# Optimization experiments

Hardware: AMD Instinct MI355X
Metric: run time of the kernel (lower is better)

Reference implementation:

```python
import jax, jax.numpy as jnp
import numpy as np

# dims
B, C, N, T = 8, 64, 500, 12      # batch, channels (c_in=c_out=nhid), nodes, time
H, F = 4, 64                      # nheads, nhid per head
GDEP = 2
ALPHA = 0.05                      # mixprop residual mix
LEAK = 0.2                        # leakyrelu slope in attention


def setup_inputs() -> dict:
    key = jax.random.key(0)
    ks = jax.random.split(key, 9)
    x = jax.random.normal(ks[0], (B, C, N, T), jnp.float32)
    adj = (jax.random.uniform(ks[1], (N, N)) < 0.05).astype(jnp.float32)
    # per-head GAT params stacked on head axis
    W = jax.random.normal(ks[2], (H, C, F), jnp.float32) * 0.05   # head projection
    a1 = jax.random.normal(ks[3], (H, F), jnp.float32) * 0.05     # a[:F]
    a2 = jax.random.normal(ks[4], (H, F), jnp.float32) * 0.05     # a[F:]
    # GAT output mlp: Conv2d 1x1, (H*F) -> F
    Wg = jax.random.normal(ks[5], (F, H * F), jnp.float32) * 0.05
    bg = jnp.zeros((F,), jnp.float32)
    # mixprop mlp: (GDEP+1)*C -> C
    Wm = jax.random.normal(ks[6], (C, (GDEP + 1) * C), jnp.float32) * 0.05
    bm = jnp.zeros((C,), jnp.float32)
    return {"x": x, "adj": adj, "W": W, "a1": a1, "a2": a2,
            "Wg": Wg, "bg": bg, "Wm": Wm, "bm": bm}


def _gat(h, mask, W, a1, a2, Wg, bg):
    # h: [B,C,N,T]; eval mode (dropout = identity)
    hp = jnp.transpose(h, (0, 3, 2, 1))                 # [B,T,N,C]
    Wh = jnp.einsum('btnc,hcf->bhtnf', hp, W)           # [B,H,T,N,F]
    e1 = jnp.einsum('bhtnf,hf->bhtn', Wh, a1)           # src term
    e2 = jnp.einsum('bhtnf,hf->bhtn', Wh, a2)           # dst term
    e = jax.nn.leaky_relu(e1[..., :, None] + e2[..., None, :], LEAK)  # [B,H,T,N,N]
    e = jnp.where(mask, e, jnp.float32(-9e15))
    att = jax.nn.softmax(e, axis=-1)
    hpr = jax.nn.elu(jnp.einsum('bhtnm,bhtmf->bhtnf', att, Wh))       # [B,H,T,N,F]
    # concat heads along channel dim -> [B, H*F, N, T]
    cat = jnp.transpose(hpr, (0, 1, 4, 3, 2)).reshape(B, H * F, N, T)
    # 1x1 conv mix
    return jnp.einsum('bcnt,oc->bont', cat, Wg) + bg[None, :, None, None]


def reference(x, adj, W, a1, a2, Wg, bg, Wm, bm):
    mask = (adj + jnp.eye(N, dtype=adj.dtype)) > 0      # self-loops added
    h = x
    outs = [h]
    for _ in range(GDEP):
        h = ALPHA * x + (1.0 - ALPHA) * _gat(h, mask, W, a1, a2, Wg, bg)
        outs.append(h)
    ho = jnp.concatenate(outs, axis=1)                  # [B,(GDEP+1)*C,N,T]
    return jnp.einsum('bcnt,oc->bont', ho, Wm) + bm[None, :, None, None]
```

## Files before the change

### kernel.cpp

```cpp
#include <hip/hip_runtime.h>
#include <hip/hip_bf16.h>
#include <math.h>

#define BB 8
#define CC 64
#define NN 500
#define TT 12
#define HH 4
#define FF 64
#define CT (CC*TT)
#define HF (HH*FF)
#define NBT (HH*TT)
#define NBHT (BB*NBT)
#define NROWS (BB*HH*TT*NN)
#define NNODE (BB*NN)
#define BSR 200
#define KST 68

typedef unsigned short ushort_t;
typedef unsigned int uint_t;
typedef __attribute__((ext_vector_type(8))) short short8;
typedef __attribute__((ext_vector_type(4))) float floatx4;

static __device__ __forceinline__ ushort_t f2bf(float v) {
    __hip_bfloat16 h = __float2bfloat16(v);
    ushort_t u;
    __builtin_memcpy(&u, &h, 2);
    return u;
}

static __device__ __forceinline__ uint_t pkbf(float a, float b) {
    __hip_bfloat162 h = __float22bfloat162_rn(make_float2(a, b));
    uint_t u;
    __builtin_memcpy(&u, &h, 4);
    return u;
}

__global__ __launch_bounds__(256) void k016_setup(const float* __restrict__ adj,
                                                  const float* __restrict__ W,
                                                  const float* __restrict__ a1,
                                                  const float* __restrict__ a2,
                                                  const float* __restrict__ Wm,
                                                  const float* __restrict__ Wg,
                                                  const float* __restrict__ x,
                                                  uint_t* __restrict__ maskbits,
                                                  float* __restrict__ p1,
                                                  float* __restrict__ p2,
                                                  ushort_t* __restrict__ WmB,
                                                  ushort_t* __restrict__ WgB,
                                                  ushort_t* __restrict__ WtB,
                                                  float* __restrict__ xT) {
    __shared__ float tile[16*776];
    int blk = blockIdx.x;
    if (blk < 32) {
        int idx = blk * 256 + threadIdx.x;
        int n = idx >> 4, j = idx & 15;
        uint_t v = 0;
        if (n < NN) {
            int m0 = j * 32;
            for (int i = 0; i < 32; ++i) {
                int m = m0 + i;
                bool p = (m < NN) && (adj[n*NN + m] > 0.f || m == n);
                v |= (p ? 1u : 0u) << i;
            }
        }
        maskbits[idx] = v;
        return;
    }
    if (blk < 209) {
        int idx = (blk - 32) * 256 + threadIdx.x;
        if (idx < HH*CC) {
            int h = idx / CC, c = idx % CC;
            float s1 = 0.f, s2 = 0.f;
            for (int f = 0; f < FF; ++f) {
                float w = W[(h*CC + c)*FF + f];
                s1 += w * a1[h*FF + f];
                s2 += w * a2[h*FF + f];
            }
            p1[idx] = s1; p2[idx] = s2;
        }
        int j = idx - HH*CC;
        if (j >= 0 && j < CC*3*CC) {
            WmB[j] = f2bf(Wm[j]);
        }
        int j2 = idx - (HH*CC + CC*3*CC);
        if (j2 >= 0 && j2 < FF*HF) {
            WgB[j2] = f2bf(Wg[j2]);
        }
        int j3 = idx - (HH*CC + CC*3*CC + FF*HF);
        if (j3 >= 0 && j3 < HH*CC*FF) {
            int h = j3 >> 12, rem = j3 & 4095;
            int f = rem >> 6, c = rem & 63;
            WtB[j3] = f2bf(W[h*4096 + c*64 + f]);
        }
        return;
    }
    int xblk = blk - 209;
    int b  = xblk >> 5;
    int n0 = (xblk & 31) * 16;
    for (int idx = threadIdx.x; idx < CC*16*TT; idx += 256) {
        int c   = idx / (16*TT);
        int rem = idx % (16*TT);
        int nl  = rem / TT;
        int t   = rem % TT;
        int n   = n0 + nl;
        if (n < NN)
            tile[nl*776 + c*TT + t] = x[((b*CC + c)*NN + n)*TT + t];
    }
    __syncthreads();
    for (int idx = threadIdx.x; idx < 16*CT; idx += 256) {
        int nl = idx / CT;
        int j  = idx % CT;
        int n  = n0 + nl;
        if (n < NN)
            xT[(size_t)(b*NN + n)*CT + j] = tile[nl*776 + j];
    }
}

__global__ __launch_bounds__(256) void k2_wh_e(const float* __restrict__ hin,
                                               const ushort_t* __restrict__ WtB,
                                               const float* __restrict__ p1,
                                               const float* __restrict__ p2,
                                               ushort_t* __restrict__ Wh,
                                               float* __restrict__ e1,
                                               float* __restrict__ e2) {
    __shared__ float    hL[4][CT];
    __shared__ ushort_t Bs[4][TT*KST];
    int tid  = threadIdx.x;
    int wid  = tid >> 6;
    int lane = tid & 63;
    int quad = lane >> 4;
    int r    = lane & 15;
    int node0 = blockIdx.x * 4;

    for (int u = 0; u < 4; ++u) {
        const float4* src = (const float4*)(hin + (size_t)(node0 + u) * CT);
        float4* dst = (float4*)hL[u];
        for (int i = tid; i < CT/4; i += 256) dst[i] = src[i];
    }
    __syncthreads();
    for (int e = tid; e < 4*CT; e += 256) {
        int u = e / CT, i = e % CT;
        int c = i / TT, t = i % TT;
        Bs[u][t*KST + c] = f2bf(hL[u][i]);
    }
    __syncthreads();

    short8 Afr[4][2];
    #pragma unroll
    for (int mt = 0; mt < 4; ++mt)
        #pragma unroll
        for (int kc = 0; kc < 2; ++kc)
            Afr[mt][kc] = *(const short8*)(WtB + wid*4096 +
                                           (mt*16 + r)*64 + kc*32 + quad*8);

    int rcl = r < TT ? r : TT-1;

    for (int u = 0; u < 4; ++u) {
        floatx4 C[4];
        #pragma unroll
        for (int mt = 0; mt < 4; ++mt) C[mt] = (floatx4){0.f,0.f,0.f,0.f};
        #pragma unroll
        for (int kc = 0; kc < 2; ++kc) {
            short8 bfr = *(const short8*)&Bs[u][rcl*KST + kc*32 + quad*8];
            #pragma unroll
            for (int mt = 0; mt < 4; ++mt)
                C[mt] = __builtin_amdgcn_mfma_f32_16x16x32_bf16(Afr[mt][kc], bfr, C[mt], 0, 0, 0);
        }
        if (r < TT) {
            int node = node0 + u;
            int bb = node / NN, nn = node % NN;
            size_t row = ((size_t)((bb*HH + wid)*TT + r)*NN + nn)*FF;
            #pragma unroll
            for (int mt = 0; mt < 4; ++mt) {
                int f0 = mt*16 + quad*4;
                *(uint_t*)&Wh[row + f0]     = pkbf(C[mt][0], C[mt][1]);
                *(uint_t*)&Wh[row + f0 + 2] = pkbf(C[mt][2], C[mt][3]);
            }
        }
    }

    int t2 = lane & 15;
    if (t2 < TT) {
        int h2 = lane >> 4;
        const float* hLw = hL[wid];
        float s1 = 0.f, s2 = 0.f;
        for (int c = 0; c < CC; ++c) {
            float v = hLw[c*TT + t2];
            s1 += v * p1[h2*CC + c];
            s2 += v * p2[h2*CC + c];
        }
        int node = node0 + wid;
        int bb = node / NN, nn = node % NN;
        int idx = ((bb*HH + h2)*TT + t2)*NN + nn;
        e1[idx] = s1;
        e2[idx] = s2;
    }
}

__global__ __launch_bounds__(256) void k2t(const ushort_t* __restrict__ Wh,
                                           ushort_t* __restrict__ WhT) {
    __shared__ ushort_t tile[32*512];
    int wid  = threadIdx.x >> 6;
    int lane = threadIdx.x & 63;
    int bht  = blockIdx.x >> 1;
    int fh   = blockIdx.x & 1;
    const ushort_t* src = Wh + (size_t)bht * NN * FF + fh*32;

    for (int task = wid; task < 32; task += 4) {
        int i  = task >> 2;
        int fo = task & 3;
        int m  = i*64 + lane;
        short8 v = {0,0,0,0,0,0,0,0};
        if (m < NN) v = *(const short8*)(src + m*FF + fo*8);
        #pragma unroll
        for (int j = 0; j < 8; ++j)
            tile[(fo*8 + j)*512 + m] = (ushort_t)v[j];
    }
    __syncthreads();

    ushort_t* dst = WhT + (size_t)bht * 64 * 512 + (size_t)fh*32*512;
    for (int f = wid; f < 32; f += 4) {
        short8 v = *(const short8*)&tile[f*512 + lane*8];
        *(short8*)(dst + f*512 + lane*8) = v;
    }
}

__global__ __launch_bounds__(256, 3) void k3_attn(const ushort_t* __restrict__ WhT,
                                                  const float* __restrict__ e1,
                                                  const float* __restrict__ e2,
                                                  const uint_t* __restrict__ maskbits,
                                                  ushort_t* __restrict__ hprB) {
    __shared__ float  e2s[512];
    __shared__ uint_t mks[256*17];
    int tid  = threadIdx.x;
    int wid  = tid >> 6;
    int lane = tid & 63;
    int bht  = blockIdx.x >> 1;
    int half = blockIdx.x & 1;
    int b    = bht / NBT;
    int ht   = bht % NBT;

    const float* e1p = e1 + (size_t)bht * NN;
    const float* e2p = e2 + (size_t)bht * NN;
    const ushort_t* WT = WhT + (size_t)bht * 64 * 512;
    const float L2E = 1.4426950408889634f;

    {
        int i = tid;
        e2s[i] = (i < NN) ? e2p[i] * L2E : 0.f;
        i = tid + 256;
        e2s[i] = (i < NN) ? e2p[i] * L2E : 0.f;
    }
    for (int i = tid; i < 256*16; i += 256) {
        int rl = i >> 4, dw = i & 15;
        mks[rl*17 + dw] = maskbits[(half*256 + rl)*16 + dw];
    }
    __syncthreads();

    int quad = lane >> 4;
    int r    = lane & 15;

    const short8 ONES = {0x3F80,0x3F80,0x3F80,0x3F80,
                         0x3F80,0x3F80,0x3F80,0x3F80};

    float e1v[4];
    #pragma unroll
    for (int u = 0; u < 4; ++u) {
        int nrow = half*256 + (wid*4 + u)*16 + r;
        e1v[u] = ((nrow < NN) ? e1p[nrow] : 0.f) * L2E;
    }
    int rl0 = wid*64 + r;

    const ushort_t* WTr = WT + (size_t)r * 512;

    floatx4 C[4][4];
    floatx4 Cs[4];
    #pragma unroll
    for (int u = 0; u < 4; ++u) {
        Cs[u] = (floatx4){0.f,0.f,0.f,0.f};
        #pragma unroll
        for (int ft = 0; ft < 4; ++ft) C[u][ft] = (floatx4){0.f,0.f,0.f,0.f};
    }

    #pragma unroll
    for (int ki = 0; ki < 16; ++ki) {
        int kb = ki*32 + quad*8;

        short8 b0 = *(const short8*)(WTr + 0*8192 + kb);
        short8 b1 = *(const short8*)(WTr + 1*8192 + kb);
        short8 b2 = *(const short8*)(WTr + 2*8192 + kb);
        short8 b3 = *(const short8*)(WTr + 3*8192 + kb);

        float4 ea = *(const float4*)&e2s[kb];
        float4 eb = *(const float4*)&e2s[kb + 4];
        float ev[8] = {ea.x,ea.y,ea.z,ea.w, eb.x,eb.y,eb.z,eb.w};

        #pragma unroll
        for (int u = 0; u < 4; ++u) {
            uint_t md    = mks[(rl0 + u*16)*17 + ki];
            uint_t mbits = md >> (quad*8);
            union { uint_t w[4]; short8 s; } av;
            #pragma unroll
            for (int p = 0; p < 4; ++p) {
                float s0 = e1v[u] + ev[2*p];
                float s1 = e1v[u] + ev[2*p+1];
                float g0 = fmaxf(s0, 0.2f*s0);
                float g1 = fmaxf(s1, 0.2f*s1);
                float x0 = __builtin_amdgcn_exp2f(g0);
                float x1 = __builtin_amdgcn_exp2f(g1);
                x0 = (mbits & (1u << (2*p)))     ? x0 : 0.f;
                x1 = (mbits & (1u << (2*p + 1))) ? x1 : 0.f;
                av.w[p] = pkbf(x0, x1);
            }
            C[u][0] = __builtin_amdgcn_mfma_f32_16x16x32_bf16(av.s, b0, C[u][0], 0, 0, 0);
            C[u][1] = __builtin_amdgcn_mfma_f32_16x16x32_bf16(av.s, b1, C[u][1], 0, 0, 0);
            C[u][2] = __builtin_amdgcn_mfma_f32_16x16x32_bf16(av.s, b2, C[u][2], 0, 0, 0);
            C[u][3] = __builtin_amdgcn_mfma_f32_16x16x32_bf16(av.s, b3, C[u][3], 0, 0, 0);
            Cs[u]   = __builtin_amdgcn_mfma_f32_16x16x32_bf16(av.s, ONES, Cs[u], 0, 0, 0);
        }
    }

    #pragma unroll
    for (int u = 0; u < 4; ++u) {
        int n0 = half*256 + (wid*4 + u)*16;
        #pragma unroll
        for (int reg = 0; reg < 4; ++reg) {
            int n = n0 + quad*4 + reg;
            if (n < NN) {
                float inv = 1.0f / Cs[u][reg];
                size_t base = ((size_t)(b*NN + n)*NBT + ht)*FF;
                #pragma unroll
                for (int ft = 0; ft < 4; ++ft) {
                    float v = C[u][ft][reg] * inv;
                    v = v > 0.f ? v : __expf(v) - 1.f;
                    hprB[base + ft*16 + r] = f2bf(v);
                }
            }
        }
    }
}

__global__ __launch_bounds__(256) void k4_mfma(const ushort_t* __restrict__ hprB,
                                               const ushort_t* __restrict__ WgB,
                                               const float* __restrict__ bg,
                                               const float* __restrict__ xT,
                                               float* __restrict__ hnext) {
    __shared__ float S[4][CT];
    int wid  = threadIdx.x >> 6;
    int lane = threadIdx.x & 63;
    int quad = lane >> 4;
    int r    = lane & 15;

    short8 Afr[4][8];
    #pragma unroll
    for (int ot = 0; ot < 4; ++ot)
        #pragma unroll
        for (int kc = 0; kc < 8; ++kc)
            Afr[ot][kc] = *(const short8*)(WgB + (size_t)(ot*16 + r)*HF + kc*32 + quad*8);

    float4 bgv[4];
    #pragma unroll
    for (int ot = 0; ot < 4; ++ot)
        bgv[ot] = *(const float4*)(bg + ot*16 + quad*4);

    int tcl = r < TT ? r : TT-1;

    int node = blockIdx.x*4 + wid;
    const ushort_t* P = hprB + (size_t)node * (NBT*FF);

    floatx4 C[4];
    #pragma unroll
    for (int ot = 0; ot < 4; ++ot) C[ot] = (floatx4){0.f,0.f,0.f,0.f};

    #pragma unroll
    for (int kc = 0; kc < 8; ++kc) {
        int k = kc*32 + quad*8;
        int h = k >> 6, f0 = k & 63;
        short8 bfr = *(const short8*)(P + (h*TT + tcl)*FF + f0);
        #pragma unroll
        for (int ot = 0; ot < 4; ++ot)
            C[ot] = __builtin_amdgcn_mfma_f32_16x16x32_bf16(Afr[ot][kc], bfr, C[ot], 0, 0, 0);
    }

    if (r < TT) {
        #pragma unroll
        for (int ot = 0; ot < 4; ++ot) {
            #pragma unroll
            for (int reg = 0; reg < 4; ++reg) {
                int o = ot*16 + quad*4 + reg;
                S[wid][o*TT + r] = C[ot][reg] + bgv[ot][reg];
            }
        }
    }
    {
        const float4* xp4 = (const float4*)(xT + (size_t)node * CT);
        float4* ho4 = (float4*)(hnext + (size_t)node * CT);
        const float4* S4 = (const float4*)S[wid];
        #pragma unroll
        for (int j = 0; j < 3; ++j) {
            int i = lane + j*64;
            float4 xv = xp4[i];
            float4 sv = S4[i];
            float4 ov;
            ov.x = 0.05f*xv.x + 0.95f*sv.x;
            ov.y = 0.05f*xv.y + 0.95f*sv.y;
            ov.z = 0.05f*xv.z + 0.95f*sv.z;
            ov.w = 0.05f*xv.w + 0.95f*sv.w;
            ho4[i] = ov;
        }
    }
}

__global__ __launch_bounds__(256) void k45_fused(const ushort_t* __restrict__ hprB,
                                                 const ushort_t* __restrict__ WgB,
                                                 const float* __restrict__ bg,
                                                 const float* __restrict__ xT,
                                                 const float* __restrict__ h1,
                                                 const ushort_t* __restrict__ WmB,
                                                 const float* __restrict__ bm,
                                                 float* __restrict__ out) {
    __shared__ ushort_t Bs[4][TT*BSR];
    __shared__ float    So[4][CT];
    int wid  = threadIdx.x >> 6;
    int lane = threadIdx.x & 63;
    int quad = lane >> 4;
    int r    = lane & 15;

    int node = blockIdx.x*4 + wid;
    ushort_t* Bw = Bs[wid];

    {
        const float* xp = xT + (size_t)node*CT + lane*TT;
        const float* hp = h1 + (size_t)node*CT + lane*TT;
        float4 x0 = *(const float4*)(xp);
        float4 x1 = *(const float4*)(xp + 4);
        float4 x2 = *(const float4*)(xp + 8);
        float4 g0 = *(const float4*)(hp);
        float4 g1 = *(const float4*)(hp + 4);
        float4 g2 = *(const float4*)(hp + 8);
        float xa[12] = {x0.x,x0.y,x0.z,x0.w, x1.x,x1.y,x1.z,x1.w,
                        x2.x,x2.y,x2.z,x2.w};
        float ha[12] = {g0.x,g0.y,g0.z,g0.w, g1.x,g1.y,g1.z,g1.w,
                        g2.x,g2.y,g2.z,g2.w};
        #pragma unroll
        for (int t = 0; t < TT; ++t) {
            Bw[t*BSR + lane]      = f2bf(xa[t]);
            Bw[t*BSR + 64 + lane] = f2bf(ha[t]);
        }
    }

    {
        short8 Afr[4][8];
        #pragma unroll
        for (int ot = 0; ot < 4; ++ot)
            #pragma unroll
            for (int kc = 0; kc < 8; ++kc)
                Afr[ot][kc] = *(const short8*)(WgB + (size_t)(ot*16 + r)*HF + kc*32 + quad*8);
        float4 bgv[4];
        #pragma unroll
        for (int ot = 0; ot < 4; ++ot)
            bgv[ot] = *(const float4*)(bg + ot*16 + quad*4);

        int tcl = r < TT ? r : TT-1;
        const ushort_t* P = hprB + (size_t)node * (NBT*FF);

        floatx4 C[4];
        #pragma unroll
        for (int ot = 0; ot < 4; ++ot) C[ot] = (floatx4){0.f,0.f,0.f,0.f};
        #pragma unroll
        for (int kc = 0; kc < 8; ++kc) {
            int k = kc*32 + quad*8;
            int h = k >> 6, f0 = k & 63;
            short8 bfr = *(const short8*)(P + (h*TT + tcl)*FF + f0);
            #pragma unroll
            for (int ot = 0; ot < 4; ++ot)
                C[ot] = __builtin_amdgcn_mfma_f32_16x16x32_bf16(Afr[ot][kc], bfr, C[ot], 0, 0, 0);
        }

        if (r < TT) {
            const float* xp = xT + (size_t)node * CT;
            #pragma unroll
            for (int ot = 0; ot < 4; ++ot) {
                #pragma unroll
                for (int rp = 0; rp < 4; rp += 2) {
                    int o = ot*16 + quad*4 + rp;
                    float v0 = C[ot][rp]   + bgv[ot][rp];
                    float v1 = C[ot][rp+1] + bgv[ot][rp+1];
                    float h20 = 0.05f*xp[o*TT + r]       + 0.95f*v0;
                    float h21 = 0.05f*xp[(o+1)*TT + r]   + 0.95f*v1;
                    *(uint_t*)&Bw[r*BSR + 128 + o] = pkbf(h20, h21);
                }
            }
        }
    }

    {
        short8 Am[4][6];
        #pragma unroll
        for (int ot = 0; ot < 4; ++ot)
            #pragma unroll
            for (int kc = 0; kc < 6; ++kc)
                Am[ot][kc] = *(const short8*)(WmB + (size_t)(ot*16 + r)*(3*CC) + kc*32 + quad*8);

        int trd = r < TT ? r : TT-1;
        floatx4 C2[4];
        #pragma unroll
        for (int ot = 0; ot < 4; ++ot) C2[ot] = (floatx4){0.f,0.f,0.f,0.f};
        #pragma unroll
        for (int kc = 0; kc < 6; ++kc) {
            short8 bfr = *(const short8*)&Bw[trd*BSR + kc*32 + quad*8];
            #pragma unroll
            for (int ot = 0; ot < 4; ++ot)
                C2[ot] = __builtin_amdgcn_mfma_f32_16x16x32_bf16(Am[ot][kc], bfr, C2[ot], 0, 0, 0);
        }

        if (r < TT) {
            #pragma unroll
            for (int ot = 0; ot < 4; ++ot) {
                float4 bmv = *(const float4*)(bm + ot*16 + quad*4);
                #pragma unroll
                for (int reg = 0; reg < 4; ++reg) {
                    int o = ot*16 + quad*4 + reg;
                    So[wid][o*TT + r] = C2[ot][reg] + bmv[reg];
                }
            }
        }
    }
    __syncthreads();

    {
        int o = threadIdx.x >> 2;
        int q = threadIdx.x & 3;
        int nodeq = blockIdx.x*4 + q;
        int bq = nodeq / NN, nq = nodeq % NN;
        float* op = out + ((size_t)(bq*CC + o)*NN + nq)*TT;
        const float* Sp = So[q] + o*TT;
        *(float4*)&op[0] = *(const float4*)&Sp[0];
        *(float4*)&op[4] = *(const float4*)&Sp[4];
        *(float4*)&op[8] = *(const float4*)&Sp[8];
    }
}

extern "C" void kernel_launch(void* const* d_in, const int* in_sizes, int n_in,
                              void* d_out, int out_size, void* d_ws, size_t ws_size,
                              hipStream_t stream) {
    const float* x   = (const float*)d_in[0];
    const float* adj = (const float*)d_in[1];
    const float* W   = (const float*)d_in[2];
    const float* a1  = (const float*)d_in[3];
    const float* a2  = (const float*)d_in[4];
    const float* Wg  = (const float*)d_in[5];
    const float* bg  = (const float*)d_in[6];
    const float* Wm  = (const float*)d_in[7];
    const float* bm  = (const float*)d_in[8];
    float* out = (float*)d_out;

    char* ws = (char*)d_ws;
    size_t off = 0;
    auto alloc = [&](size_t bytes) -> void* {
        void* p = ws + off;
        off += (bytes + 255) & ~(size_t)255;
        return p;
    };

    uint_t* maskbits = (uint_t*)alloc((size_t)512 * 16 * 4);
    float* p1   = (float*)alloc(HH*CC * sizeof(float));
    float* p2   = (float*)alloc(HH*CC * sizeof(float));
    ushort_t* WmB = (ushort_t*)alloc((size_t)CC*3*CC * 2);
    ushort_t* WgB = (ushort_t*)alloc((size_t)FF*HF * 2);
    ushort_t* WtB = (ushort_t*)alloc((size_t)HH*CC*FF * 2);
    float* xT   = (float*)alloc((size_t)NNODE * CT * sizeof(float));
    ushort_t* Wh   = (ushort_t*)alloc((size_t)NROWS * FF * 2);
    ushort_t* WhT  = (ushort_t*)alloc((size_t)NBHT * 64 * 512 * 2);
    ushort_t* hprB = (ushort_t*)alloc((size_t)NNODE * NBT * FF * 2);
    float* e1   = (float*)alloc((size_t)NROWS * sizeof(float));
    float* e2   = (float*)alloc((size_t)NROWS * sizeof(float));
    float* h1   = (float*)alloc((size_t)NNODE * CT * sizeof(float));
    (void)ws_size;

    k016_setup<<<465, 256, 0, stream>>>(adj, W, a1, a2, Wm, Wg, x,
                                        maskbits, p1, p2, WmB, WgB, WtB, xT);

    k2_wh_e <<<NNODE/4, 256, 0, stream>>>(xT, WtB, p1, p2, Wh, e1, e2);
    k2t     <<<NBHT*2,  256, 0, stream>>>(Wh, WhT);
    k3_attn <<<NBHT*2,  256, 0, stream>>>(WhT, e1, e2, maskbits, hprB);
    k4_mfma <<<NNODE/4, 256, 0, stream>>>(hprB, WgB, bg, xT, h1);

    k2_wh_e <<<NNODE/4, 256, 0, stream>>>(h1, WtB, p1, p2, Wh, e1, e2);
    k2t     <<<NBHT*2,  256, 0, stream>>>(Wh, WhT);
    k3_attn <<<NBHT*2,  256, 0, stream>>>(WhT, e1, e2, maskbits, hprB);

    k45_fused<<<NNODE/4, 256, 0, stream>>>(hprB, WgB, bg, xT, h1, WmB, bm, out);
}
```

Before: 304.8 us.

## Fuse Wh transpose into projection kernel, writing transposed WhT directly

The projection kernel now handles 8 nodes per block within one batch and stages its MFMA results in shared memory in transposed [t][f][node] order. It then writes 16-byte chunks straight into the node-contiguous WhT layout, so the separate k2t transpose kernel and the intermediate Wh buffer are gone. This removes one launch and a global round trip of Wh per GAT layer. The setup kernel zeroes the WhT padding columns (500..511) once. In exchange, shared-memory use per block grows and the e1/e2 dot products are moved before the MFMA phase.

After: 303.2 us. No clear change (-0.5%).

```diff
diff --git a/kernel.cpp b/kernel.cpp
--- a/kernel.cpp
+++ b/kernel.cpp
@@ -16,6 +16,7 @@
 #define NNODE (BB*NN)
 #define BSR 200
 #define KST 68
+#define WTS 520
 
 typedef unsigned short ushort_t;
 typedef unsigned int uint_t;
@@ -49,7 +50,8 @@
                                                   ushort_t* __restrict__ WmB,
                                                   ushort_t* __restrict__ WgB,
                                                   ushort_t* __restrict__ WtB,
-                                                  float* __restrict__ xT) {
+                                                  float* __restrict__ xT,
+                                                  ushort_t* __restrict__ WhT) {
     __shared__ float tile[16*776];
     int blk = blockIdx.x;
     if (blk < 32) {
@@ -95,6 +97,13 @@
         }
         return;
     }
+    if (blk >= 465) {
+        int row = (blk - 465) * 256 + threadIdx.x;
+        uint_t* p = (uint_t*)(WhT + (size_t)row * 512 + 500);
+        #pragma unroll
+        for (int j = 0; j < 6; ++j) p[j] = 0;
+        return;
+    }
     int xblk = blk - 209;
     int b  = xblk >> 5;
     int n0 = (xblk & 31) * 16;
@@ -121,30 +130,56 @@
                                                const ushort_t* __restrict__ WtB,
                                                const float* __restrict__ p1,
                                                const float* __restrict__ p2,
-                                               ushort_t* __restrict__ Wh,
+                                               ushort_t* __restrict__ WhT,
                                                float* __restrict__ e1,
                                                float* __restrict__ e2) {
-    __shared__ float    hL[4][CT];
-    __shared__ ushort_t Bs[4][TT*KST];
+    __shared__ char uni[4*TT*WTS*2];
+    __shared__ ushort_t Bs[8][TT*KST];
+    float (*hL)[CT] = (float(*)[CT])uni;
     int tid  = threadIdx.x;
     int wid  = tid >> 6;
     int lane = tid & 63;
     int quad = lane >> 4;
     int r    = lane & 15;
-    int node0 = blockIdx.x * 4;
-
-    for (int u = 0; u < 4; ++u) {
-        const float4* src = (const float4*)(hin + (size_t)(node0 + u) * CT);
-        float4* dst = (float4*)hL[u];
-        for (int i = tid; i < CT/4; i += 256) dst[i] = src[i];
+    int b    = blockIdx.x / 63;
+    int nl0  = (blockIdx.x % 63) * 8;
+
+    for (int i = tid; i < 8*(CT/4); i += 256) {
+        int u = i / (CT/4), j = i % (CT/4);
+        int node = b*NN + nl0 + u;
+        if (node > NNODE-1) node = NNODE-1;
+        ((float4*)hL[u])[j] = ((const float4*)(hin + (size_t)node*CT))[j];
     }
     __syncthreads();
-    for (int e = tid; e < 4*CT; e += 256) {
+    for (int e = tid; e < 8*CT; e += 256) {
         int u = e / CT, i = e % CT;
         int c = i / TT, t = i % TT;
         Bs[u][t*KST + c] = f2bf(hL[u][i]);
     }
+    {
+        int t2 = lane & 15, h2 = lane >> 4;
+        if (t2 < TT) {
+            for (int pass = 0; pass < 2; ++pass) {
+                int u  = wid + pass*4;
+                int nl = nl0 + u;
+                if (nl < NN) {
+                    const float* hLw = hL[u];
+                    float s1 = 0.f, s2 = 0.f;
+                    for (int c = 0; c < CC; ++c) {
+                        float v = hLw[c*TT + t2];
+                        s1 += v * p1[h2*CC + c];
+                        s2 += v * p2[h2*CC + c];
+                    }
+                    int idx = ((b*HH + h2)*TT + t2)*NN + nl;
+                    e1[idx] = s1;
+                    e2[idx] = s2;
+                }
+            }
+        }
+    }
     __syncthreads();
+
+    ushort_t* WTl = (ushort_t*)uni + wid*(TT*WTS);
 
     short8 Afr[4][2];
     #pragma unroll
@@ -156,7 +191,8 @@
 
     int rcl = r < TT ? r : TT-1;
 
-    for (int u = 0; u < 4; ++u) {
+    for (int u = 0; u < 8; ++u) {
+        bool valid = (nl0 + u) < NN;
         floatx4 C[4];
         #pragma unroll
         for (int mt = 0; mt < 4; ++mt) C[mt] = (floatx4){0.f,0.f,0.f,0.f};
@@ -168,61 +204,24 @@
                 C[mt] = __builtin_amdgcn_mfma_f32_16x16x32_bf16(Afr[mt][kc], bfr, C[mt], 0, 0, 0);
         }
         if (r < TT) {
-            int node = node0 + u;
-            int bb = node / NN, nn = node % NN;
-            size_t row = ((size_t)((bb*HH + wid)*TT + r)*NN + nn)*FF;
             #pragma unroll
             for (int mt = 0; mt < 4; ++mt) {
-                int f0 = mt*16 + quad*4;
-                *(uint_t*)&Wh[row + f0]     = pkbf(C[mt][0], C[mt][1]);
-                *(uint_t*)&Wh[row + f0 + 2] = pkbf(C[mt][2], C[mt][3]);
-            }
-        }
-    }
-
-    int t2 = lane & 15;
-    if (t2 < TT) {
-        int h2 = lane >> 4;
-        const float* hLw = hL[wid];
-        float s1 = 0.f, s2 = 0.f;
-        for (int c = 0; c < CC; ++c) {
-            float v = hLw[c*TT + t2];
-            s1 += v * p1[h2*CC + c];
-            s2 += v * p2[h2*CC + c];
-        }
-        int node = node0 + wid;
-        int bb = node / NN, nn = node % NN;
-        int idx = ((bb*HH + h2)*TT + t2)*NN + nn;
-        e1[idx] = s1;
-        e2[idx] = s2;
-    }
-}
-
-__global__ __launch_bounds__(256) void k2t(const ushort_t* __restrict__ Wh,
-                                           ushort_t* __restrict__ WhT) {
-    __shared__ ushort_t tile[32*512];
-    int wid  = threadIdx.x >> 6;
-    int lane = threadIdx.x & 63;
-    int bht  = blockIdx.x >> 1;
-    int fh   = blockIdx.x & 1;
-    const ushort_t* src = Wh + (size_t)bht * NN * FF + fh*32;
-
-    for (int task = wid; task < 32; task += 4) {
-        int i  = task >> 2;
-        int fo = task & 3;
-        int m  = i*64 + lane;
-        short8 v = {0,0,0,0,0,0,0,0};
-        if (m < NN) v = *(const short8*)(src + m*FF + fo*8);
-        #pragma unroll
-        for (int j = 0; j < 8; ++j)
-            tile[(fo*8 + j)*512 + m] = (ushort_t)v[j];
-    }
-    __syncthreads();
-
-    ushort_t* dst = WhT + (size_t)bht * 64 * 512 + (size_t)fh*32*512;
-    for (int f = wid; f < 32; f += 4) {
-        short8 v = *(const short8*)&tile[f*512 + lane*8];
-        *(short8*)(dst + f*512 + lane*8) = v;
+                #pragma unroll
+                for (int reg = 0; reg < 4; ++reg) {
+                    int f = mt*16 + quad*4 + reg;
+                    WTl[r*WTS + f*8 + u] = valid ? f2bf(C[mt][reg]) : (ushort_t)0;
+                }
+            }
+        }
+    }
+
+    {
+        size_t base = ((size_t)(b*NBT + wid*TT) * 64) * 512 + nl0;
+        #pragma unroll
+        for (int t = 0; t < TT; ++t) {
+            short8 v = *(const short8*)&WTl[t*WTS + lane*8];
+            *(short8*)(WhT + base + ((size_t)t*64 + lane)*512) = v;
+        }
     }
 }
 
@@ -571,7 +570,6 @@
     ushort_t* WgB = (ushort_t*)alloc((size_t)FF*HF * 2);
     ushort_t* WtB = (ushort_t*)alloc((size_t)HH*CC*FF * 2);
     float* xT   = (float*)alloc((size_t)NNODE * CT * sizeof(float));
-    ushort_t* Wh   = (ushort_t*)alloc((size_t)NROWS * FF * 2);
     ushort_t* WhT  = (ushort_t*)alloc((size_t)NBHT * 64 * 512 * 2);
     ushort_t* hprB = (ushort_t*)alloc((size_t)NNODE * NBT * FF * 2);
     float* e1   = (float*)alloc((size_t)NROWS * sizeof(float));
@@ -579,16 +577,14 @@
     float* h1   = (float*)alloc((size_t)NNODE * CT * sizeof(float));
     (void)ws_size;
 
-    k016_setup<<<465, 256, 0, stream>>>(adj, W, a1, a2, Wm, Wg, x,
-                                        maskbits, p1, p2, WmB, WgB, WtB, xT);
-
-    k2_wh_e <<<NNODE/4, 256, 0, stream>>>(xT, WtB, p1, p2, Wh, e1, e2);
-    k2t     <<<NBHT*2,  256, 0, stream>>>(Wh, WhT);
+    k016_setup<<<561, 256, 0, stream>>>(adj, W, a1, a2, Wm, Wg, x,
+                                        maskbits, p1, p2, WmB, WgB, WtB, xT, WhT);
+
+    k2_wh_e <<<8*63,    256, 0, stream>>>(xT, WtB, p1, p2, WhT, e1, e2);
     k3_attn <<<NBHT*2,  256, 0, stream>>>(WhT, e1, e2, maskbits, hprB);
     k4_mfma <<<NNODE/4, 256, 0, stream>>>(hprB, WgB, bg, xT, h1);
 
-    k2_wh_e <<<NNODE/4, 256, 0, stream>>>(h1, WtB, p1, p2, Wh, e1, e2);
-    k2t     <<<NBHT*2,  256, 0, stream>>>(Wh, WhT);
+    k2_wh_e <<<8*63,    256, 0, stream>>>(h1, WtB, p1, p2, WhT, e1, e2);
     k3_attn <<<NBHT*2,  256, 0, stream>>>(WhT, e1, e2, maskbits, hprB);
 
     k45_fused<<<NNODE/4, 256, 0, stream>>>(hprB, WgB, bg, xT, h1, WmB, bm, out);
```
